# Kernel tuning notes

Hardware: AMD Instinct MI355X
Metric: run time of the kernel (lower is better)

## Reference

```python
import jax, jax.numpy as jnp
import numpy as np

INPUT_DIM, HIDDEN_DIM, N_HEADS, N_AGENTS = 256, 512, 8, 64
BATCH, N_ENTITIES = 128, 256


def setup_inputs() -> dict:
    key = jax.random.key(0)
    ks = jax.random.split(key, 6)
    x = jax.random.normal(ks[0], (BATCH, N_ENTITIES, INPUT_DIM), dtype=jnp.float32)
    # encode: LeakyReLU -> Linear(input_dim, hidden_dim)
    W_enc = jax.random.normal(ks[1], (INPUT_DIM, HIDDEN_DIM), dtype=jnp.float32) * (1.0 / np.sqrt(INPUT_DIM))
    b_enc = jnp.zeros((HIDDEN_DIM,), dtype=jnp.float32)
    # per-head full hidden x hidden projections, stacked on head axis
    WQ = jax.random.normal(ks[2], (N_HEADS, HIDDEN_DIM, HIDDEN_DIM), dtype=jnp.float32)
    WK = jax.random.normal(ks[3], (N_HEADS, HIDDEN_DIM, HIDDEN_DIM), dtype=jnp.float32)
    WV = jax.random.normal(ks[4], (N_HEADS, HIDDEN_DIM, HIDDEN_DIM), dtype=jnp.float32)
    return {"x": x, "W_enc": W_enc, "b_enc": b_enc, "WQ": WQ, "WK": WK, "WV": WV, "n_agents": N_AGENTS}


def reference(x, W_enc, b_enc, WQ, WK, WV, n_agents):
    scale = 1.0 / np.sqrt(WQ.shape[-1]).astype(np.float32)
    # encode: LeakyReLU(0.01) then Linear
    h = jax.nn.leaky_relu(x, negative_slope=0.01) @ W_enc + b_enc  # [b, e, H]
    ha = h[:, :n_agents]  # [b, a, H]
    # all heads at once: n = head axis
    Q = jnp.einsum('bah,nhd->nbad', ha, WQ)
    K = jnp.einsum('beh,nhd->nbed', h, WK)
    V = jnp.einsum('beh,nhd->nbed', h, WV)
    scores = jnp.einsum('nbad,nbed->nbae', Q, K) * scale
    p = jax.nn.softmax(scores, axis=-1)
    # redundant renormalization from the original code
    prob = p / (jnp.sum(p, axis=-1, keepdims=True) + 1e-12)
    z = jnp.einsum('nbae,nbed->nbad', prob, V)  # [n, b, a, H]
    return jnp.mean(z, axis=0)  # [b, a, H]
```

## Files before the change

kernel.cpp:

```cpp
#include <hip/hip_runtime.h>
#include <math.h>

#define BATCH  128
#define NENT   256
#define INDIM  256
#define HID    512
#define NHEAD  8
#define NAGENT 64
#define SCALE  0.04419417382415922f


typedef unsigned short u16;
typedef unsigned int   u32;

typedef __bf16 bf16x8  __attribute__((ext_vector_type(8)));
typedef float  floatx4 __attribute__((ext_vector_type(4)));
typedef u32    u32x4   __attribute__((ext_vector_type(4)));
typedef u32    u32x2   __attribute__((ext_vector_type(2)));

union Frag {
    u32x4 s;
    struct { u32x2 lo, hi; } p;
    bf16x8 v;
};

__device__ __forceinline__ u16 f2bf(float x) {
    u32 u = __float_as_uint(x);
    return (u16)((u + 0x7FFFu + ((u >> 16) & 1u)) >> 16);
}
__device__ __forceinline__ float bf2f(u16 b) {
    return __uint_as_float(((u32)b) << 16);
}
__device__ __forceinline__ void split4(const float4& r, ushort4& hh, ushort4& hl) {
    hh.x = f2bf(r.x); hl.x = f2bf(r.x - bf2f(hh.x));
    hh.y = f2bf(r.y); hl.y = f2bf(r.y - bf2f(hh.y));
    hh.z = f2bf(r.z); hl.z = f2bf(r.z - bf2f(hh.z));
    hh.w = f2bf(r.w); hl.w = f2bf(r.w - bf2f(hh.w));
}

__global__ __launch_bounds__(256) void wenc_t_kernel(const float* __restrict__ W,
                                                     u16* __restrict__ Wt_p) {
    __shared__ float tile[64][68];
    const int bid = blockIdx.x;
    const int k0 = (bid & 3) * 64;
    const int d0 = (bid >> 2) * 64;
    const int t = threadIdx.x;
    const int ki = t >> 2, dc = (t & 3) * 16;
    #pragma unroll
    for (int c = 0; c < 4; ++c)
        *(float4*)&tile[ki][dc + c * 4] =
            *(const float4*)(W + (size_t)(k0 + ki) * HID + d0 + dc + c * 4);
    __syncthreads();
    const int dr = t >> 2, kc = (t & 3) * 16;
    #pragma unroll
    for (int c = 0; c < 4; ++c) {
        float4 v = make_float4(tile[kc + c * 4 + 0][dr], tile[kc + c * 4 + 1][dr],
                               tile[kc + c * 4 + 2][dr], tile[kc + c * 4 + 3][dr]);
        ushort4 hh, hl; split4(v, hh, hl);
        const int kk = k0 + kc + c * 4;
        size_t o = (size_t)(d0 + dr) * 512 + (size_t)(kk >> 5) * 64 + (kk & 31);
        *(ushort4*)(Wt_p + o) = hh;
        *(ushort4*)(Wt_p + o + 32) = hl;
    }
}

__global__ __launch_bounds__(256) void enc_kernel(const float* __restrict__ x,
                                                  const u16* __restrict__ Wt_p,
                                                  const float* __restrict__ bias,
                                                  u16* __restrict__ h_p) {
    __shared__ u16 Ah[32][264];
    __shared__ u16 Al[32][264];
    const int r0 = blockIdx.x * 32;
    const int t  = threadIdx.x;
    {
        const int row = t >> 3;
        const float* xr = x + (size_t)(r0 + row) * INDIM;
        #pragma unroll
        for (int j = 0; j < 8; ++j) {
            const int k0 = ((t & 7) + j * 8) * 4;
            float4 v = *(const float4*)(xr + k0);
            v.x = v.x > 0.f ? v.x : 0.01f * v.x;
            v.y = v.y > 0.f ? v.y : 0.01f * v.y;
            v.z = v.z > 0.f ? v.z : 0.01f * v.z;
            v.w = v.w > 0.f ? v.w : 0.01f * v.w;
            ushort4 hh, hl; split4(v, hh, hl);
            *(ushort4*)&Ah[row][k0] = hh;
            *(ushort4*)&Al[row][k0] = hl;
        }
    }
    __syncthreads();

    const int wid = t >> 6, lane = t & 63, l15 = lane & 15, quad = lane >> 4;
    const int mbase = (wid & 1) * 16;
    const int nbase = (wid >> 1) * 256;
    const floatx4 z4 = {0.f, 0.f, 0.f, 0.f};
    floatx4 acc[16];
    #pragma unroll
    for (int i = 0; i < 16; ++i) acc[i] = z4;

    for (int ks = 0; ks < 8; ++ks) {
        const int k = ks * 32 + quad * 8;
        Frag Afh, Afl;
        Afh.s = *(const u32x4*)&Ah[mbase + l15][k];
        Afl.s = *(const u32x4*)&Al[mbase + l15][k];
        #pragma unroll
        for (int nt = 0; nt < 16; ++nt) {
            const int d = nbase + nt * 16 + l15;
            const size_t wo = (size_t)d * 512 + (size_t)ks * 64 + quad * 8;
            Frag Bh, Bl;
            Bh.s = *(const u32x4*)(Wt_p + wo);
            Bl.s = *(const u32x4*)(Wt_p + wo + 32);
            floatx4 c = acc[nt];
            c = __builtin_amdgcn_mfma_f32_16x16x32_bf16(Afh.v, Bh.v, c, 0, 0, 0);
            c = __builtin_amdgcn_mfma_f32_16x16x32_bf16(Afh.v, Bl.v, c, 0, 0, 0);
            c = __builtin_amdgcn_mfma_f32_16x16x32_bf16(Afl.v, Bh.v, c, 0, 0, 0);
            acc[nt] = c;
        }
    }
    #pragma unroll
    for (int nt = 0; nt < 16; ++nt) {
        const int d = nbase + nt * 16 + l15;
        const float bv = bias[d];
        #pragma unroll
        for (int r = 0; r < 4; ++r) {
            const float v = acc[nt][r] + bv;
            const u16 hi = f2bf(v);
            const u16 lo = f2bf(v - bf2f(hi));
            const size_t o = (size_t)(r0 + mbase + quad * 4 + r) * 1024
                           + (size_t)(d >> 5) * 64 + (d & 31);
            h_p[o]      = hi;
            h_p[o + 32] = lo;
        }
    }
}

__global__ __launch_bounds__(256) void ht_kernel(const u16* __restrict__ h_p,
                                                 u16* __restrict__ hT) {
    __shared__ u16 tile[64][72];
    const int bid = blockIdx.x;
    const int dt = bid & 7;
    const int et = (bid >> 3) & 3;
    const int b  = bid >> 5;
    const int t  = threadIdx.x;
    const int r  = t >> 2, cs = (t & 3) * 16;
    const int dg = dt * 64 + cs;
    const u16* src = h_p + (size_t)(b * 256 + et * 64 + r) * 1024
                   + (size_t)(dg >> 5) * 64 + (dg & 31);
    *(ushort4*)&tile[r][cs + 0]  = *(const ushort4*)(src + 0);
    *(ushort4*)&tile[r][cs + 4]  = *(const ushort4*)(src + 4);
    *(ushort4*)&tile[r][cs + 8]  = *(const ushort4*)(src + 8);
    *(ushort4*)&tile[r][cs + 12] = *(const ushort4*)(src + 12);
    __syncthreads();
    const int d = t >> 2, es = (t & 3) * 16;
    u16* dst = hT + (size_t)b * 131072 + (size_t)(dt * 64 + d) * 256 + et * 64 + es;
    #pragma unroll
    for (int c = 0; c < 4; ++c) {
        ushort4 v = make_ushort4(tile[es + c * 4 + 0][d], tile[es + c * 4 + 1][d],
                                 tile[es + c * 4 + 2][d], tile[es + c * 4 + 3][d]);
        *(ushort4*)(dst + c * 4) = v;
    }
}

__global__ __launch_bounds__(256) void wqk_kernel(const float* __restrict__ WQ,
                                                  const float* __restrict__ WK,
                                                  u16* __restrict__ Mt_p) {
    __shared__ u16 Ah[64][72], Al[64][72], Bh[64][72], Bl[64][72];
    const int bid = blockIdx.x;
    const int jt = (bid & 7) * 64;
    const int it = ((bid >> 3) & 7) * 64;
    const int n  = bid >> 6;
    const float* qp = WQ + (size_t)n * 262144;
    const float* kp = WK + (size_t)n * 262144;
    const int t = threadIdx.x;
    const int wid = t >> 6, lane = t & 63, l15 = lane & 15, quad = lane >> 4;
    const int srow = t >> 2, sc = (t & 3) * 16;

    const floatx4 z4 = {0.f, 0.f, 0.f, 0.f};
    floatx4 acc[4];
    #pragma unroll
    for (int i = 0; i < 4; ++i) acc[i] = z4;

    for (int kc = 0; kc < HID; kc += 64) {
        #pragma unroll
        for (int f = 0; f < 4; ++f) {
            float4 va = *(const float4*)(kp + (size_t)(jt + srow) * HID + kc + sc + f * 4);
            ushort4 hh, hl; split4(va, hh, hl);
            *(ushort4*)&Ah[srow][sc + f * 4] = hh;
            *(ushort4*)&Al[srow][sc + f * 4] = hl;
            float4 vb = *(const float4*)(qp + (size_t)(it + srow) * HID + kc + sc + f * 4);
            split4(vb, hh, hl);
            *(ushort4*)&Bh[srow][sc + f * 4] = hh;
            *(ushort4*)&Bl[srow][sc + f * 4] = hl;
        }
        __syncthreads();
        #pragma unroll
        for (int ks = 0; ks < 2; ++ks) {
            const int k = ks * 32 + quad * 8;
            Frag Afh, Afl;
            Afh.s = *(const u32x4*)&Ah[wid * 16 + l15][k];
            Afl.s = *(const u32x4*)&Al[wid * 16 + l15][k];
            #pragma unroll
            for (int nt = 0; nt < 4; ++nt) {
                Frag Bfh, Bfl;
                Bfh.s = *(const u32x4*)&Bh[nt * 16 + l15][k];
                Bfl.s = *(const u32x4*)&Bl[nt * 16 + l15][k];
                floatx4 c = acc[nt];
                c = __builtin_amdgcn_mfma_f32_16x16x32_bf16(Afh.v, Bfh.v, c, 0, 0, 0);
                c = __builtin_amdgcn_mfma_f32_16x16x32_bf16(Afh.v, Bfl.v, c, 0, 0, 0);
                c = __builtin_amdgcn_mfma_f32_16x16x32_bf16(Afl.v, Bfh.v, c, 0, 0, 0);
                acc[nt] = c;
            }
        }
        __syncthreads();
    }
    #pragma unroll
    for (int nt = 0; nt < 4; ++nt)
        #pragma unroll
        for (int r = 0; r < 4; ++r) {
            const float v = acc[nt][r] * SCALE;
            const u16 hi = f2bf(v);
            const u16 lo = f2bf(v - bf2f(hi));
            const int j = jt + wid * 16 + quad * 4 + r;
            const int i = it + nt * 16 + l15;
            const size_t o = (size_t)n * 524288 + (size_t)j * 1024
                           + (size_t)(i >> 5) * 64 + (i & 31);
            Mt_p[o]      = hi;
            Mt_p[o + 32] = lo;
        }
}

__global__ __launch_bounds__(256) void wvt_kernel(const float* __restrict__ WV,
                                                  u16* __restrict__ WVt) {
    __shared__ float tile[64][68];
    const int bid = blockIdx.x;
    const int i0 = (bid & 7) * 64;
    const int o0 = ((bid >> 3) & 7) * 64;
    const int n  = bid >> 6;
    const float* src = WV + (size_t)n * 262144;
    const int t  = threadIdx.x;
    const int di = t >> 2;
    const int dc = (t & 3) * 16;
    #pragma unroll
    for (int c = 0; c < 4; ++c)
        *(float4*)&tile[di][dc + c * 4] =
            *(const float4*)(src + (size_t)(i0 + di) * HID + o0 + dc + c * 4);
    __syncthreads();
    const int dr = t >> 2;
    const int ic = (t & 3) * 16;
    size_t o = (size_t)n * 262144 + (size_t)(o0 + dr) * HID + i0 + ic;
    #pragma unroll
    for (int c = 0; c < 4; ++c) {
        ushort4 v = make_ushort4(f2bf(tile[ic + c * 4 + 0][dr]), f2bf(tile[ic + c * 4 + 1][dr]),
                                 f2bf(tile[ic + c * 4 + 2][dr]), f2bf(tile[ic + c * 4 + 3][dr]));
        *(ushort4*)(WVt + o + c * 4) = v;
    }
}

template<bool USE_HT>
__global__ __launch_bounds__(256, 3) void attn_kernel(const u16* __restrict__ h_p,
                                                      const u16* __restrict__ Mt_p,
                                                      const u16* __restrict__ WVt,
                                                      const u16* __restrict__ hT,
                                                      float* __restrict__ out) {
    __shared__ __align__(16) char SM[53504];
    u16*   Th  = (u16*)SM;
    u16*   Tl  = (u16*)(SM + 16640);
    float* S   = (float*)SM;
    float* red = (float*)(SM + 33792);
    u16*   HbT = (u16*)SM;
    u16*   U   = (u16*)SM;
    u16*   Pt  = (u16*)(SM + 36864);

    const int bid = blockIdx.x;
    const int x7 = bid & 7;
    const int s  = bid >> 3;
    const int at = s & 1;
    const int n  = (x7 >> 1) | (((s >> 1) & 1) << 2);
    const int b  = ((s >> 2) << 1) | (x7 & 1);

    const int tid  = threadIdx.x;
    const int wid  = tid >> 6;
    const int lane = tid & 63;
    const int l15  = lane & 15;
    const int quad = lane >> 4;

    const u16* Mtp = Mt_p + (size_t)n * 524288;
    const u16* Wv  = WVt  + (size_t)n * 262144;
    const u16* hTb = hT + (size_t)b * 131072;
    const size_t hb_base = (size_t)b * 262144;
    const size_t ha_row0 = hb_base + (size_t)(at * 32) * 1024;

    const floatx4 z4 = {0.f, 0.f, 0.f, 0.f};
    floatx4 Sacc[8];
    #pragma unroll
    for (int i = 0; i < 8; ++i) Sacc[i] = z4;

    for (int H = 0; H < 2; ++H) {
        floatx4 Tacc[8];
        #pragma unroll
        for (int i = 0; i < 8; ++i) Tacc[i] = z4;
        for (int ks = 0; ks < 16; ++ks) {
            const int ko = ks * 64 + quad * 8;
            Frag Ahf[2], Alf[2];
            #pragma unroll
            for (int mt = 0; mt < 2; ++mt) {
                const size_t ro = ha_row0 + (size_t)(mt * 16 + l15) * 1024 + ko;
                Ahf[mt].s = *(const u32x4*)(h_p + ro);
                Alf[mt].s = *(const u32x4*)(h_p + ro + 32);
            }
            #pragma unroll
            for (int nt = 0; nt < 4; ++nt) {
                const int d = H * 256 + (wid * 4 + nt) * 16 + l15;
                const size_t mo = (size_t)d * 1024 + ko;
                Frag Bh, Bl;
                Bh.s = *(const u32x4*)(Mtp + mo);
                Bl.s = *(const u32x4*)(Mtp + mo + 32);
                #pragma unroll
                for (int mt = 0; mt < 2; ++mt) {
                    floatx4 c = Tacc[mt * 4 + nt];
                    c = __builtin_amdgcn_mfma_f32_16x16x32_bf16(Ahf[mt].v, Bh.v, c, 0, 0, 0);
                    c = __builtin_amdgcn_mfma_f32_16x16x32_bf16(Ahf[mt].v, Bl.v, c, 0, 0, 0);
                    c = __builtin_amdgcn_mfma_f32_16x16x32_bf16(Alf[mt].v, Bh.v, c, 0, 0, 0);
                    Tacc[mt * 4 + nt] = c;
                }
            }
        }
        __syncthreads();
        #pragma unroll
        for (int mt = 0; mt < 2; ++mt)
            #pragma unroll
            for (int nt = 0; nt < 4; ++nt)
                #pragma unroll
                for (int r = 0; r < 4; ++r) {
                    const float v = Tacc[mt * 4 + nt][r];
                    const int a  = mt * 16 + quad * 4 + r;
                    const int dl = (wid * 4 + nt) * 16 + l15;
                    const u16 hi = f2bf(v);
                    Th[a * 260 + dl] = hi;
                    Tl[a * 260 + dl] = f2bf(v - bf2f(hi));
                }
        __syncthreads();
        for (int ks = 0; ks < 8; ++ks) {
            const int kl = ks * 32 + quad * 8;
            const int ko = (H * 8 + ks) * 64 + quad * 8;
            Frag Ahf[4], Alf[4];
            #pragma unroll
            for (int mt = 0; mt < 4; ++mt) {
                const size_t ro = hb_base + (size_t)((wid * 4 + mt) * 16 + l15) * 1024 + ko;
                Ahf[mt].s = *(const u32x4*)(h_p + ro);
                Alf[mt].s = *(const u32x4*)(h_p + ro + 32);
            }
            #pragma unroll
            for (int nt = 0; nt < 2; ++nt) {
                const int ac = nt * 16 + l15;
                Frag Bfh, Bfl;
                Bfh.p.lo = *(const u32x2*)(Th + ac * 260 + kl);
                Bfh.p.hi = *(const u32x2*)(Th + ac * 260 + kl + 4);
                Bfl.p.lo = *(const u32x2*)(Tl + ac * 260 + kl);
                Bfl.p.hi = *(const u32x2*)(Tl + ac * 260 + kl + 4);
                #pragma unroll
                for (int mt = 0; mt < 4; ++mt) {
                    floatx4 c = Sacc[mt * 2 + nt];
                    c = __builtin_amdgcn_mfma_f32_16x16x32_bf16(Ahf[mt].v, Bfh.v, c, 0, 0, 0);
                    c = __builtin_amdgcn_mfma_f32_16x16x32_bf16(Ahf[mt].v, Bfl.v, c, 0, 0, 0);
                    c = __builtin_amdgcn_mfma_f32_16x16x32_bf16(Alf[mt].v, Bfh.v, c, 0, 0, 0);
                    Sacc[mt * 2 + nt] = c;
                }
            }
        }
    }
    __syncthreads();
    #pragma unroll
    for (int mt = 0; mt < 4; ++mt)
        #pragma unroll
        for (int nt = 0; nt < 2; ++nt)
            #pragma unroll
            for (int r = 0; r < 4; ++r) {
                const int e = (wid * 4 + mt) * 16 + quad * 4 + r;
                const int a = nt * 16 + l15;
                S[e * 33 + a] = Sacc[mt * 2 + nt][r];
            }
    __syncthreads();
    {
        const int a   = tid & 31;
        const int seg = tid >> 5;
        float v[32];
        #pragma unroll
        for (int i = 0; i < 32; ++i) v[i] = S[(seg * 32 + i) * 33 + a];
        float mx = v[0];
        #pragma unroll
        for (int i = 1; i < 32; ++i) mx = fmaxf(mx, v[i]);
        red[a * 8 + seg] = mx;
        __syncthreads();
        float gmx = red[a * 8 + 0];
        #pragma unroll
        for (int i = 1; i < 8; ++i) gmx = fmaxf(gmx, red[a * 8 + i]);
        __syncthreads();
        float sum = 0.f;
        #pragma unroll
        for (int i = 0; i < 32; ++i) { v[i] = expf(v[i] - gmx); sum += v[i]; }
        red[a * 8 + seg] = sum;
        __syncthreads();
        float tot = 0.f;
        #pragma unroll
        for (int i = 0; i < 8; ++i) tot += red[a * 8 + i];
        const float inv = 1.0f / tot;
        #pragma unroll
        for (int i = 0; i < 32; ++i)
            Pt[a * 260 + seg * 32 + i] = f2bf(v[i] * inv);
    }
    __syncthreads();
    floatx4 Uacc[16];
    #pragma unroll
    for (int i = 0; i < 16; ++i) Uacc[i] = z4;
    const int d0w = wid * 128;
    if (USE_HT) {
        for (int ep = 0; ep < 4; ++ep) {
            Frag Bc[2][8];
            #pragma unroll
            for (int sb = 0; sb < 2; ++sb)
                #pragma unroll
                for (int dt = 0; dt < 8; ++dt) {
                    const int d = d0w + dt * 16 + l15;
                    Bc[sb][dt].s = *(const u32x4*)(hTb + (size_t)d * 256
                                                   + (2 * ep + sb) * 32 + quad * 8);
                }
            #pragma unroll
            for (int sb = 0; sb < 2; ++sb) {
                const int et = 2 * ep + sb;
                Frag Ap[2];
                #pragma unroll
                for (int mt = 0; mt < 2; ++mt) {
                    const int ar = mt * 16 + l15;
                    Ap[mt].p.lo = *(const u32x2*)(Pt + ar * 260 + et * 32 + quad * 8);
                    Ap[mt].p.hi = *(const u32x2*)(Pt + ar * 260 + et * 32 + quad * 8 + 4);
                }
                #pragma unroll
                for (int dt = 0; dt < 8; ++dt)
                    #pragma unroll
                    for (int mt = 0; mt < 2; ++mt)
                        Uacc[mt * 8 + dt] = __builtin_amdgcn_mfma_f32_16x16x32_bf16(
                            Ap[mt].v, Bc[sb][dt].v, Uacc[mt * 8 + dt], 0, 0, 0);
            }
        }
    } else {
        u32* Hb32 = (u32*)HbT;
        for (int et = 0; et < 8; ++et) {
            {
                const int epi = lane & 15;
                const int q   = lane >> 4;
                const size_t r0p = hb_base + (size_t)(et * 32 + 2 * epi) * 1024;
                #pragma unroll
                for (int c = 0; c < 4; ++c) {
                    const int d0 = d0w + c * 32 + q * 8;
                    const size_t po = (size_t)(d0 >> 5) * 64 + (d0 & 31);
                    u32x4 u0 = *(const u32x4*)(h_p + r0p + po);
                    u32x4 u1 = *(const u32x4*)(h_p + r0p + 1024 + po);
                    #pragma unroll
                    for (int p = 0; p < 4; ++p) {
                        const u32 w0 = (u0[p] & 0xFFFFu) | (u1[p] << 16);
                        const u32 w1 = (u0[p] >> 16) | (u1[p] & 0xFFFF0000u);
                        Hb32[(d0 + 2 * p) * 18 + epi]     = w0;
                        Hb32[(d0 + 2 * p + 1) * 18 + epi] = w1;
                    }
                }
            }
            Frag Ap[2];
            #pragma unroll
            for (int mt = 0; mt < 2; ++mt) {
                const int ar = mt * 16 + l15;
                Ap[mt].p.lo = *(const u32x2*)(Pt + ar * 260 + et * 32 + quad * 8);
                Ap[mt].p.hi = *(const u32x2*)(Pt + ar * 260 + et * 32 + quad * 8 + 4);
            }
            #pragma unroll
            for (int dt = 0; dt < 8; ++dt) {
                const int d = d0w + dt * 16 + l15;
                Frag Bf;
                Bf.p.lo = *(const u32x2*)(HbT + d * 36 + quad * 8);
                Bf.p.hi = *(const u32x2*)(HbT + d * 36 + quad * 8 + 4);
                #pragma unroll
                for (int mt = 0; mt < 2; ++mt)
                    Uacc[mt * 8 + dt] = __builtin_amdgcn_mfma_f32_16x16x32_bf16(
                        Ap[mt].v, Bf.v, Uacc[mt * 8 + dt], 0, 0, 0);
            }
        }
    }
    __syncthreads();
    #pragma unroll
    for (int mt = 0; mt < 2; ++mt)
        #pragma unroll
        for (int dt = 0; dt < 8; ++dt)
            #pragma unroll
            for (int r = 0; r < 4; ++r) {
                const int a = mt * 16 + quad * 4 + r;
                const int d = d0w + dt * 16 + l15;
                U[a * 520 + d] = f2bf(Uacc[mt * 8 + dt][r]);
            }
    __syncthreads();
    floatx4 Zacc[16];
    #pragma unroll
    for (int i = 0; i < 16; ++i) Zacc[i] = z4;
    for (int kp = 0; kp < 8; ++kp) {
        Frag Bw[2][8];
        #pragma unroll
        for (int sb = 0; sb < 2; ++sb) {
            const int k = (kp * 2 + sb) * 32 + quad * 8;
            #pragma unroll
            for (int dt = 0; dt < 8; ++dt) {
                const int dn = (wid * 8 + dt) * 16 + l15;
                Bw[sb][dt].s = *(const u32x4*)(Wv + (size_t)dn * HID + k);
            }
        }
        #pragma unroll
        for (int sb = 0; sb < 2; ++sb) {
            const int k = (kp * 2 + sb) * 32 + quad * 8;
            Frag Au[2];
            #pragma unroll
            for (int mt = 0; mt < 2; ++mt) {
                Au[mt].p.lo = *(const u32x2*)(U + (mt * 16 + l15) * 520 + k);
                Au[mt].p.hi = *(const u32x2*)(U + (mt * 16 + l15) * 520 + k + 4);
            }
            #pragma unroll
            for (int dt = 0; dt < 8; ++dt)
                #pragma unroll
                for (int mt = 0; mt < 2; ++mt)
                    Zacc[mt * 8 + dt] = __builtin_amdgcn_mfma_f32_16x16x32_bf16(
                        Au[mt].v, Bw[sb][dt].v, Zacc[mt * 8 + dt], 0, 0, 0);
        }
    }
    float* ob = out + ((size_t)b * NAGENT + at * 32) * HID;
    #pragma unroll
    for (int mt = 0; mt < 2; ++mt)
        #pragma unroll
        for (int dt = 0; dt < 8; ++dt)
            #pragma unroll
            for (int r = 0; r < 4; ++r) {
                const int a  = mt * 16 + quad * 4 + r;
                const int dn = (wid * 8 + dt) * 16 + l15;
                atomicAdd(ob + (size_t)a * HID + dn, Zacc[mt * 8 + dt][r] * 0.125f);
            }
}

extern "C" void kernel_launch(void* const* d_in, const int* in_sizes, int n_in,
                              void* d_out, int out_size, void* d_ws, size_t ws_size,
                              hipStream_t stream) {
    const float* x     = (const float*)d_in[0];
    const float* W_enc = (const float*)d_in[1];
    const float* b_enc = (const float*)d_in[2];
    const float* WQ    = (const float*)d_in[3];
    const float* WK    = (const float*)d_in[4];
    const float* WV    = (const float*)d_in[5];
    float* out = (float*)d_out;

    char* ws = (char*)d_ws;
    u16* h_p  = (u16*)ws;
    u16* Mt_p = (u16*)(ws + 67108864);
    u16* WVt  = (u16*)(ws + 75497472);
    u16* hT   = (u16*)(ws + 79691776);
    u16* Wt_p = WVt;

    const bool useHT = ws_size >= (size_t)113246208;

    hipMemsetAsync(d_out, 0, (size_t)out_size * sizeof(float), stream);
    wenc_t_kernel<<<32, 256, 0, stream>>>(W_enc, Wt_p);
    enc_kernel<<<1024, 256, 0, stream>>>(x, Wt_p, b_enc, h_p);
    if (useHT) ht_kernel<<<4096, 256, 0, stream>>>(h_p, hT);
    wvt_kernel<<<512, 256, 0, stream>>>(WV, WVt);
    wqk_kernel<<<512, 256, 0, stream>>>(WQ, WK, Mt_p);
    if (useHT)
        attn_kernel<true><<<2048, 256, 0, stream>>>(h_p, Mt_p, WVt, hT, out);
    else
        attn_kernel<false><<<2048, 256, 0, stream>>>(h_p, Mt_p, WVt, hT, out);
}
```

Baseline: 967.1 us.

## Store operands in MFMA-fragment chunk layout and double-buffer via global_load_lds

Intermediate buffers (h, M^T, W_V, h^T) are rewritten in a 16-row chunked layout that matches MFMA fragment order, so each fragment load becomes a contiguous 16-byte access. The attention kernel now streams B operands into per-wave LDS staging buffers with global_load_lds in a double-buffered pipeline using waitcnt, and splits the T and U stages into quarters to fit LDS. The goal is to cut strided global loads and hide memory latency, at the cost of more LDS pressure, more barriers and more complex index math.

```diff
diff --git a/kernel.cpp b/kernel.cpp
--- a/kernel.cpp
+++ b/kernel.cpp
@@ -24,6 +24,15 @@
     bf16x8 v;
 };
 
+#define MFMA(a, b, c) __builtin_amdgcn_mfma_f32_16x16x32_bf16((a), (b), (c), 0, 0, 0)
+#define VMW(n) (((n) & 0xF) | (0xF << 8) | (0x7 << 4))
+
+__device__ __forceinline__ void gld16(const u16* g, u16* l) {
+    __builtin_amdgcn_global_load_lds(
+        (const __attribute__((address_space(1))) void*)g,
+        (__attribute__((address_space(3))) void*)l, 16, 0, 0);
+}
+
 __device__ __forceinline__ u16 f2bf(float x) {
     u32 u = __float_as_uint(x);
     return (u16)((u + 0x7FFFu + ((u >> 16) & 1u)) >> 16);
@@ -36,6 +45,9 @@
     hh.y = f2bf(r.y); hl.y = f2bf(r.y - bf2f(hh.y));
     hh.z = f2bf(r.z); hl.z = f2bf(r.z - bf2f(hh.z));
     hh.w = f2bf(r.w); hl.w = f2bf(r.w - bf2f(hh.w));
+}
+__device__ __forceinline__ size_t chunk_off(int row16, int col) {
+    return (size_t)((col >> 3) & 3) * 128 + (size_t)row16 * 8 + (col & 7);
 }
 
 __global__ __launch_bounds__(256) void wenc_t_kernel(const float* __restrict__ W,
@@ -67,7 +79,7 @@
 __global__ __launch_bounds__(256) void enc_kernel(const float* __restrict__ x,
                                                   const u16* __restrict__ Wt_p,
                                                   const float* __restrict__ bias,
-                                                  u16* __restrict__ h_p) {
+                                                  u16* __restrict__ hC) {
     __shared__ u16 Ah[32][264];
     __shared__ u16 Al[32][264];
     const int r0 = blockIdx.x * 32;
@@ -111,9 +123,9 @@
             Bh.s = *(const u32x4*)(Wt_p + wo);
             Bl.s = *(const u32x4*)(Wt_p + wo + 32);
             floatx4 c = acc[nt];
-            c = __builtin_amdgcn_mfma_f32_16x16x32_bf16(Afh.v, Bh.v, c, 0, 0, 0);
-            c = __builtin_amdgcn_mfma_f32_16x16x32_bf16(Afh.v, Bl.v, c, 0, 0, 0);
-            c = __builtin_amdgcn_mfma_f32_16x16x32_bf16(Afl.v, Bh.v, c, 0, 0, 0);
+            c = MFMA(Afh.v, Bh.v, c);
+            c = MFMA(Afh.v, Bl.v, c);
+            c = MFMA(Afl.v, Bh.v, c);
             acc[nt] = c;
         }
     }
@@ -126,44 +138,49 @@
             const float v = acc[nt][r] + bv;
             const u16 hi = f2bf(v);
             const u16 lo = f2bf(v - bf2f(hi));
-            const size_t o = (size_t)(r0 + mbase + quad * 4 + r) * 1024
-                           + (size_t)(d >> 5) * 64 + (d & 31);
-            h_p[o]      = hi;
-            h_p[o + 32] = lo;
-        }
-    }
-}
-
-__global__ __launch_bounds__(256) void ht_kernel(const u16* __restrict__ h_p,
-                                                 u16* __restrict__ hT) {
+            const int row = r0 + mbase + quad * 4 + r;
+            const size_t o = (size_t)((row >> 4) * 16 + (d >> 5)) * 1024
+                           + chunk_off(row & 15, d);
+            hC[o]       = hi;
+            hC[o + 512] = lo;
+        }
+    }
+}
+
+__global__ __launch_bounds__(256) void ht_kernel(const u16* __restrict__ hC,
+                                                 u16* __restrict__ hTC) {
     __shared__ u16 tile[64][72];
     const int bid = blockIdx.x;
-    const int dt = bid & 7;
-    const int et = (bid >> 3) & 3;
-    const int b  = bid >> 5;
-    const int t  = threadIdx.x;
+    const int dt64 = bid & 7;
+    const int et64 = (bid >> 3) & 3;
+    const int b    = bid >> 5;
+    const int t    = threadIdx.x;
     const int r  = t >> 2, cs = (t & 3) * 16;
-    const int dg = dt * 64 + cs;
-    const u16* src = h_p + (size_t)(b * 256 + et * 64 + r) * 1024
-                   + (size_t)(dg >> 5) * 64 + (dg & 31);
-    *(ushort4*)&tile[r][cs + 0]  = *(const ushort4*)(src + 0);
-    *(ushort4*)&tile[r][cs + 4]  = *(const ushort4*)(src + 4);
-    *(ushort4*)&tile[r][cs + 8]  = *(const ushort4*)(src + 8);
-    *(ushort4*)&tile[r][cs + 12] = *(const ushort4*)(src + 12);
+    const int row = b * 256 + et64 * 64 + r;
+    #pragma unroll
+    for (int c = 0; c < 4; ++c) {
+        const int d0 = dt64 * 64 + cs + c * 4;
+        const size_t o = (size_t)((row >> 4) * 16 + (d0 >> 5)) * 1024
+                       + chunk_off(row & 15, d0);
+        *(ushort4*)&tile[r][cs + c * 4] = *(const ushort4*)(hC + o);
+    }
     __syncthreads();
-    const int d = t >> 2, es = (t & 3) * 16;
-    u16* dst = hT + (size_t)b * 131072 + (size_t)(dt * 64 + d) * 256 + et * 64 + es;
+    const int dr = t >> 2, es = (t & 3) * 16;
+    const int dg = dt64 * 64 + dr;
     #pragma unroll
     for (int c = 0; c < 4; ++c) {
-        ushort4 v = make_ushort4(tile[es + c * 4 + 0][d], tile[es + c * 4 + 1][d],
-                                 tile[es + c * 4 + 2][d], tile[es + c * 4 + 3][d]);
-        *(ushort4*)(dst + c * 4) = v;
+        const int e = et64 * 64 + es + c * 4;
+        ushort4 v = make_ushort4(tile[es + c * 4 + 0][dr], tile[es + c * 4 + 1][dr],
+                                 tile[es + c * 4 + 2][dr], tile[es + c * 4 + 3][dr]);
+        const size_t o = (size_t)((b * 32 + (dg >> 4)) * 8 + (e >> 5)) * 512
+                       + (size_t)((e >> 3) & 3) * 128 + (size_t)(dg & 15) * 8 + (e & 7);
+        *(ushort4*)(hTC + o) = v;
     }
 }
 
 __global__ __launch_bounds__(256) void wqk_kernel(const float* __restrict__ WQ,
                                                   const float* __restrict__ WK,
-                                                  u16* __restrict__ Mt_p) {
+                                                  u16* __restrict__ MtC) {
     __shared__ u16 Ah[64][72], Al[64][72], Bh[64][72], Bl[64][72];
     const int bid = blockIdx.x;
     const int jt = (bid & 7) * 64;
@@ -205,9 +222,9 @@
                 Bfh.s = *(const u32x4*)&Bh[nt * 16 + l15][k];
                 Bfl.s = *(const u32x4*)&Bl[nt * 16 + l15][k];
                 floatx4 c = acc[nt];
-                c = __builtin_amdgcn_mfma_f32_16x16x32_bf16(Afh.v, Bfh.v, c, 0, 0, 0);
-                c = __builtin_amdgcn_mfma_f32_16x16x32_bf16(Afh.v, Bfl.v, c, 0, 0, 0);
-                c = __builtin_amdgcn_mfma_f32_16x16x32_bf16(Afl.v, Bfh.v, c, 0, 0, 0);
+                c = MFMA(Afh.v, Bfh.v, c);
+                c = MFMA(Afh.v, Bfl.v, c);
+                c = MFMA(Afl.v, Bfh.v, c);
                 acc[nt] = c;
             }
         }
@@ -222,15 +239,16 @@
             const u16 lo = f2bf(v - bf2f(hi));
             const int j = jt + wid * 16 + quad * 4 + r;
             const int i = it + nt * 16 + l15;
-            const size_t o = (size_t)n * 524288 + (size_t)j * 1024
-                           + (size_t)(i >> 5) * 64 + (i & 31);
-            Mt_p[o]      = hi;
-            Mt_p[o + 32] = lo;
+            const size_t o = (size_t)n * 524288
+                           + (size_t)((j >> 4) * 16 + (i >> 5)) * 1024
+                           + chunk_off(j & 15, i);
+            MtC[o]       = hi;
+            MtC[o + 512] = lo;
         }
 }
 
 __global__ __launch_bounds__(256) void wvt_kernel(const float* __restrict__ WV,
-                                                  u16* __restrict__ WVt) {
+                                                  u16* __restrict__ WvC) {
     __shared__ float tile[64][68];
     const int bid = blockIdx.x;
     const int i0 = (bid & 7) * 64;
@@ -247,29 +265,31 @@
     __syncthreads();
     const int dr = t >> 2;
     const int ic = (t & 3) * 16;
-    size_t o = (size_t)n * 262144 + (size_t)(o0 + dr) * HID + i0 + ic;
+    const int dn = o0 + dr;
     #pragma unroll
     for (int c = 0; c < 4; ++c) {
+        const int k = i0 + ic + c * 4;
         ushort4 v = make_ushort4(f2bf(tile[ic + c * 4 + 0][dr]), f2bf(tile[ic + c * 4 + 1][dr]),
                                  f2bf(tile[ic + c * 4 + 2][dr]), f2bf(tile[ic + c * 4 + 3][dr]));
-        *(ushort4*)(WVt + o + c * 4) = v;
+        const size_t o = (size_t)((n * 32 + (dn >> 4)) * 16 + (k >> 5)) * 512
+                       + (size_t)((k >> 3) & 3) * 128 + (size_t)(dn & 15) * 8 + (k & 7);
+        *(ushort4*)(WvC + o) = v;
     }
 }
 
 template<bool USE_HT>
-__global__ __launch_bounds__(256, 3) void attn_kernel(const u16* __restrict__ h_p,
-                                                      const u16* __restrict__ Mt_p,
-                                                      const u16* __restrict__ WVt,
-                                                      const u16* __restrict__ hT,
+__global__ __launch_bounds__(256, 3) void attn_kernel(const u16* __restrict__ hC,
+                                                      const u16* __restrict__ MtC_g,
+                                                      const u16* __restrict__ WvC_g,
+                                                      const u16* __restrict__ hTC,
                                                       float* __restrict__ out) {
     __shared__ __align__(16) char SM[53504];
-    u16*   Th  = (u16*)SM;
-    u16*   Tl  = (u16*)(SM + 16640);
     float* S   = (float*)SM;
     float* red = (float*)(SM + 33792);
+    u16*   Uq  = (u16*)(SM + 34816);
+    u16*   Tq  = (u16*)(SM + 36864);
+    u16*   Pt  = (u16*)(SM + 36864);
     u16*   HbT = (u16*)SM;
-    u16*   U   = (u16*)SM;
-    u16*   Pt  = (u16*)(SM + 36864);
 
     const int bid = blockIdx.x;
     const int x7 = bid & 7;
@@ -284,92 +304,136 @@
     const int l15  = lane & 15;
     const int quad = lane >> 4;
 
-    const u16* Mtp = Mt_p + (size_t)n * 524288;
-    const u16* Wv  = WVt  + (size_t)n * 262144;
-    const u16* hTb = hT + (size_t)b * 131072;
-    const size_t hb_base = (size_t)b * 262144;
-    const size_t ha_row0 = hb_base + (size_t)(at * 32) * 1024;
+    u16* stg = (u16*)(SM + wid * 8192);
+
+    const u16* MtC = MtC_g + (size_t)n * 524288;
+    const u16* WvC = WvC_g + (size_t)n * 262144;
+    const int  rtA = b * 16 + at * 2;
 
     const floatx4 z4 = {0.f, 0.f, 0.f, 0.f};
     floatx4 Sacc[8];
     #pragma unroll
     for (int i = 0; i < 8; ++i) Sacc[i] = z4;
 
-    for (int H = 0; H < 2; ++H) {
-        floatx4 Tacc[8];
-        #pragma unroll
-        for (int i = 0; i < 8; ++i) Tacc[i] = z4;
+    for (int qtr = 0; qtr < 4; ++qtr) {
+        floatx4 Tacc[4] = {z4, z4, z4, z4};
+        Frag Aq[2][4];
+        auto dmaA = [&](int ks, int bsel) {
+            u16* dst = stg + bsel * 2048;
+            #pragma unroll
+            for (int nt = 0; nt < 2; ++nt) {
+                const u16* src = MtC + (size_t)((qtr * 8 + wid * 2 + nt) * 16 + ks) * 1024;
+                gld16(src + lane * 8,       dst + nt * 1024 + lane * 8);
+                gld16(src + 512 + lane * 8, dst + nt * 1024 + 512 + lane * 8);
+            }
+        };
+        auto ldA = [&](int ks, Frag* A) {
+            #pragma unroll
+            for (int mt = 0; mt < 2; ++mt) {
+                const u16* src = hC + (size_t)((rtA + mt) * 16 + ks) * 1024
+                               + quad * 128 + l15 * 8;
+                A[mt * 2 + 0].s = *(const u32x4*)src;
+                A[mt * 2 + 1].s = *(const u32x4*)(src + 512);
+            }
+        };
+        dmaA(0, 0);
+        __builtin_amdgcn_wave_barrier();
+        ldA(0, Aq[0]);
+        __builtin_amdgcn_wave_barrier();
+        #pragma unroll 2
         for (int ks = 0; ks < 16; ++ks) {
-            const int ko = ks * 64 + quad * 8;
+            const int bsel = ks & 1;
+            if (ks < 15) {
+                dmaA(ks + 1, bsel ^ 1);
+                __builtin_amdgcn_wave_barrier();
+                ldA(ks + 1, Aq[bsel ^ 1]);
+                __builtin_amdgcn_wave_barrier();
+                __builtin_amdgcn_s_waitcnt(VMW(8));
+            } else {
+                __builtin_amdgcn_s_waitcnt(VMW(0));
+            }
+            __builtin_amdgcn_wave_barrier();
+            const u16* buf = stg + bsel * 2048;
+            #pragma unroll
+            for (int nt = 0; nt < 2; ++nt) {
+                Frag Bh, Bl;
+                Bh.s = *(const u32x4*)(buf + nt * 1024 + quad * 128 + l15 * 8);
+                Bl.s = *(const u32x4*)(buf + nt * 1024 + 512 + quad * 128 + l15 * 8);
+                #pragma unroll
+                for (int mt = 0; mt < 2; ++mt) {
+                    floatx4 c = Tacc[mt * 2 + nt];
+                    c = MFMA(Aq[bsel][mt * 2 + 0].v, Bh.v, c);
+                    c = MFMA(Aq[bsel][mt * 2 + 0].v, Bl.v, c);
+                    c = MFMA(Aq[bsel][mt * 2 + 1].v, Bh.v, c);
+                    Tacc[mt * 2 + nt] = c;
+                }
+            }
+        }
+        __syncthreads();
+        #pragma unroll
+        for (int mt = 0; mt < 2; ++mt)
+            #pragma unroll
+            for (int nt = 0; nt < 2; ++nt)
+                #pragma unroll
+                for (int r = 0; r < 4; ++r) {
+                    const float v = Tacc[mt * 2 + nt][r];
+                    const int a   = mt * 16 + quad * 4 + r;
+                    const int col = (wid * 2 + nt) * 16 + l15;
+                    const u16 hi = f2bf(v);
+                    Tq[a * 260 + (col >> 5) * 64 + (col & 31)]      = hi;
+                    Tq[a * 260 + (col >> 5) * 64 + (col & 31) + 32] = f2bf(v - bf2f(hi));
+                }
+        __syncthreads();
+        auto dmaB = [&](int st, int bsel) {
+            const int ks = st >> 1, h = st & 1;
+            u16* dst = stg + bsel * 2048;
+            #pragma unroll
+            for (int i = 0; i < 2; ++i) {
+                const int rt = b * 16 + wid * 4 + h * 2 + i;
+                const u16* src = hC + (size_t)(rt * 16 + qtr * 4 + ks) * 1024;
+                gld16(src + lane * 8,       dst + i * 1024 + lane * 8);
+                gld16(src + 512 + lane * 8, dst + i * 1024 + 512 + lane * 8);
+            }
+        };
+        dmaB(0, 0);
+        #pragma unroll 2
+        for (int st = 0; st < 8; ++st) {
+            const int bsel = st & 1;
+            if (st < 7) {
+                dmaB(st + 1, bsel ^ 1);
+                __builtin_amdgcn_s_waitcnt(VMW(4));
+            } else {
+                __builtin_amdgcn_s_waitcnt(VMW(0));
+            }
+            __builtin_amdgcn_wave_barrier();
+            const int ks = st >> 1, h = st & 1;
+            const u16* buf = stg + bsel * 2048;
             Frag Ahf[2], Alf[2];
             #pragma unroll
-            for (int mt = 0; mt < 2; ++mt) {
-                const size_t ro = ha_row0 + (size_t)(mt * 16 + l15) * 1024 + ko;
-                Ahf[mt].s = *(const u32x4*)(h_p + ro);
-                Alf[mt].s = *(const u32x4*)(h_p + ro + 32);
-            }
-            #pragma unroll
-            for (int nt = 0; nt < 4; ++nt) {
-                const int d = H * 256 + (wid * 4 + nt) * 16 + l15;
-                const size_t mo = (size_t)d * 1024 + ko;
-                Frag Bh, Bl;
-                Bh.s = *(const u32x4*)(Mtp + mo);
-                Bl.s = *(const u32x4*)(Mtp + mo + 32);
-                #pragma unroll
-                for (int mt = 0; mt < 2; ++mt) {
-                    floatx4 c = Tacc[mt * 4 + nt];
-                    c = __builtin_amdgcn_mfma_f32_16x16x32_bf16(Ahf[mt].v, Bh.v, c, 0, 0, 0);
-                    c = __builtin_amdgcn_mfma_f32_16x16x32_bf16(Ahf[mt].v, Bl.v, c, 0, 0, 0);
-                    c = __builtin_amdgcn_mfma_f32_16x16x32_bf16(Alf[mt].v, Bh.v, c, 0, 0, 0);
-                    Tacc[mt * 4 + nt] = c;
-                }
-            }
-        }
-        __syncthreads();
-        #pragma unroll
-        for (int mt = 0; mt < 2; ++mt)
-            #pragma unroll
-            for (int nt = 0; nt < 4; ++nt)
-                #pragma unroll
-                for (int r = 0; r < 4; ++r) {
-                    const float v = Tacc[mt * 4 + nt][r];
-                    const int a  = mt * 16 + quad * 4 + r;
-                    const int dl = (wid * 4 + nt) * 16 + l15;
-                    const u16 hi = f2bf(v);
-                    Th[a * 260 + dl] = hi;
-                    Tl[a * 260 + dl] = f2bf(v - bf2f(hi));
-                }
-        __syncthreads();
-        for (int ks = 0; ks < 8; ++ks) {
-            const int kl = ks * 32 + quad * 8;
-            const int ko = (H * 8 + ks) * 64 + quad * 8;
-            Frag Ahf[4], Alf[4];
-            #pragma unroll
-            for (int mt = 0; mt < 4; ++mt) {
-                const size_t ro = hb_base + (size_t)((wid * 4 + mt) * 16 + l15) * 1024 + ko;
-                Ahf[mt].s = *(const u32x4*)(h_p + ro);
-                Alf[mt].s = *(const u32x4*)(h_p + ro + 32);
+            for (int i = 0; i < 2; ++i) {
+                Ahf[i].s = *(const u32x4*)(buf + i * 1024 + quad * 128 + l15 * 8);
+                Alf[i].s = *(const u32x4*)(buf + i * 1024 + 512 + quad * 128 + l15 * 8);
             }
             #pragma unroll
             for (int nt = 0; nt < 2; ++nt) {
                 const int ac = nt * 16 + l15;
                 Frag Bfh, Bfl;
-                Bfh.p.lo = *(const u32x2*)(Th + ac * 260 + kl);
-                Bfh.p.hi = *(const u32x2*)(Th + ac * 260 + kl + 4);
-                Bfl.p.lo = *(const u32x2*)(Tl + ac * 260 + kl);
-                Bfl.p.hi = *(const u32x2*)(Tl + ac * 260 + kl + 4);
-                #pragma unroll
-                for (int mt = 0; mt < 4; ++mt) {
-                    floatx4 c = Sacc[mt * 2 + nt];
-                    c = __builtin_amdgcn_mfma_f32_16x16x32_bf16(Ahf[mt].v, Bfh.v, c, 0, 0, 0);
-                    c = __builtin_amdgcn_mfma_f32_16x16x32_bf16(Ahf[mt].v, Bfl.v, c, 0, 0, 0);
-                    c = __builtin_amdgcn_mfma_f32_16x16x32_bf16(Alf[mt].v, Bfh.v, c, 0, 0, 0);
-                    Sacc[mt * 2 + nt] = c;
+                Bfh.p.lo = *(const u32x2*)(Tq + ac * 260 + ks * 64 + quad * 8);
+                Bfh.p.hi = *(const u32x2*)(Tq + ac * 260 + ks * 64 + quad * 8 + 4);
+                Bfl.p.lo = *(const u32x2*)(Tq + ac * 260 + ks * 64 + quad * 8 + 32);
+                Bfl.p.hi = *(const u32x2*)(Tq + ac * 260 + ks * 64 + quad * 8 + 36);
+                #pragma unroll
+                for (int i = 0; i < 2; ++i) {
+                    floatx4 c = Sacc[(h * 2 + i) * 2 + nt];
+                    c = MFMA(Ahf[i].v, Bfh.v, c);
+                    c = MFMA(Ahf[i].v, Bfl.v, c);
+                    c = MFMA(Alf[i].v, Bfh.v, c);
+                    Sacc[(h * 2 + i) * 2 + nt] = c;
                 }
             }
         }
-    }
-    __syncthreads();
+        __syncthreads();
+    }
     #pragma unroll
     for (int mt = 0; mt < 4; ++mt)
         #pragma unroll
@@ -415,32 +479,42 @@
     for (int i = 0; i < 16; ++i) Uacc[i] = z4;
     const int d0w = wid * 128;
     if (USE_HT) {
-        for (int ep = 0; ep < 4; ++ep) {
-            Frag Bc[2][8];
-            #pragma unroll
-            for (int sb = 0; sb < 2; ++sb)
-                #pragma unroll
-                for (int dt = 0; dt < 8; ++dt) {
-                    const int d = d0w + dt * 16 + l15;
-                    Bc[sb][dt].s = *(const u32x4*)(hTb + (size_t)d * 256
-                                                   + (2 * ep + sb) * 32 + quad * 8);
-                }
-            #pragma unroll
-            for (int sb = 0; sb < 2; ++sb) {
-                const int et = 2 * ep + sb;
-                Frag Ap[2];
-                #pragma unroll
-                for (int mt = 0; mt < 2; ++mt) {
-                    const int ar = mt * 16 + l15;
-                    Ap[mt].p.lo = *(const u32x2*)(Pt + ar * 260 + et * 32 + quad * 8);
-                    Ap[mt].p.hi = *(const u32x2*)(Pt + ar * 260 + et * 32 + quad * 8 + 4);
-                }
-                #pragma unroll
-                for (int dt = 0; dt < 8; ++dt)
-                    #pragma unroll
-                    for (int mt = 0; mt < 2; ++mt)
-                        Uacc[mt * 8 + dt] = __builtin_amdgcn_mfma_f32_16x16x32_bf16(
-                            Ap[mt].v, Bc[sb][dt].v, Uacc[mt * 8 + dt], 0, 0, 0);
+        auto dmaC = [&](int st, int bsel) {
+            const int et = st >> 1, h = st & 1;
+            u16* dst = stg + bsel * 2048;
+            #pragma unroll
+            for (int i = 0; i < 4; ++i) {
+                const u16* src = hTC + (size_t)((b * 32 + wid * 8 + h * 4 + i) * 8 + et) * 512;
+                gld16(src + lane * 8, dst + i * 512 + lane * 8);
+            }
+        };
+        dmaC(0, 0);
+        #pragma unroll 2
+        for (int st = 0; st < 16; ++st) {
+            const int bsel = st & 1;
+            if (st < 15) {
+                dmaC(st + 1, bsel ^ 1);
+                __builtin_amdgcn_s_waitcnt(VMW(4));
+            } else {
+                __builtin_amdgcn_s_waitcnt(VMW(0));
+            }
+            __builtin_amdgcn_wave_barrier();
+            const int et = st >> 1, h = st & 1;
+            const u16* buf = stg + bsel * 2048;
+            Frag Ap[2];
+            #pragma unroll
+            for (int mt = 0; mt < 2; ++mt) {
+                const int ar = mt * 16 + l15;
+                Ap[mt].p.lo = *(const u32x2*)(Pt + ar * 260 + et * 32 + quad * 8);
+                Ap[mt].p.hi = *(const u32x2*)(Pt + ar * 260 + et * 32 + quad * 8 + 4);
+            }
+            #pragma unroll
+            for (int i = 0; i < 4; ++i) {
+                Frag Bf;
+                Bf.s = *(const u32x4*)(buf + i * 512 + quad * 128 + l15 * 8);
+                #pragma unroll
+                for (int mt = 0; mt < 2; ++mt)
+                    Uacc[mt * 8 + h * 4 + i] = MFMA(Ap[mt].v, Bf.v, Uacc[mt * 8 + h * 4 + i]);
             }
         }
     } else {
@@ -448,14 +522,18 @@
         for (int et = 0; et < 8; ++et) {
             {
                 const int epi = lane & 15;
-                const int q   = lane >> 4;
-                const size_t r0p = hb_base + (size_t)(et * 32 + 2 * epi) * 1024;
+                const int q8  = lane >> 4;
                 #pragma unroll
                 for (int c = 0; c < 4; ++c) {
-                    const int d0 = d0w + c * 32 + q * 8;
-                    const size_t po = (size_t)(d0 >> 5) * 64 + (d0 & 31);
-                    u32x4 u0 = *(const u32x4*)(h_p + r0p + po);
-                    u32x4 u1 = *(const u32x4*)(h_p + r0p + 1024 + po);
+                    const int d0 = d0w + c * 32 + q8 * 8;
+                    const int row0 = et * 32 + 2 * epi;
+                    const size_t o0 = (size_t)((b * 16 + (row0 >> 4)) * 16 + (d0 >> 5)) * 1024
+                                    + chunk_off(row0 & 15, d0);
+                    const int row1 = row0 + 1;
+                    const size_t o1 = (size_t)((b * 16 + (row1 >> 4)) * 16 + (d0 >> 5)) * 1024
+                                    + chunk_off(row1 & 15, d0);
+                    u32x4 u0 = *(const u32x4*)(hC + o0);
+                    u32x4 u1 = *(const u32x4*)(hC + o1);
                     #pragma unroll
                     for (int p = 0; p < 4; ++p) {
                         const u32 w0 = (u0[p] & 0xFFFFu) | (u1[p] << 16);
@@ -480,52 +558,65 @@
                 Bf.p.hi = *(const u32x2*)(HbT + d * 36 + quad * 8 + 4);
                 #pragma unroll
                 for (int mt = 0; mt < 2; ++mt)
-                    Uacc[mt * 8 + dt] = __builtin_amdgcn_mfma_f32_16x16x32_bf16(
-                        Ap[mt].v, Bf.v, Uacc[mt * 8 + dt], 0, 0, 0);
-            }
-        }
-    }
-    __syncthreads();
-    #pragma unroll
-    for (int mt = 0; mt < 2; ++mt)
-        #pragma unroll
-        for (int dt = 0; dt < 8; ++dt)
-            #pragma unroll
-            for (int r = 0; r < 4; ++r) {
-                const int a = mt * 16 + quad * 4 + r;
-                const int d = d0w + dt * 16 + l15;
-                U[a * 520 + d] = f2bf(Uacc[mt * 8 + dt][r]);
-            }
-    __syncthreads();
+                    Uacc[mt * 8 + dt] = MFMA(Ap[mt].v, Bf.v, Uacc[mt * 8 + dt]);
+            }
+        }
+    }
     floatx4 Zacc[16];
     #pragma unroll
     for (int i = 0; i < 16; ++i) Zacc[i] = z4;
-    for (int kp = 0; kp < 8; ++kp) {
-        Frag Bw[2][8];
-        #pragma unroll
-        for (int sb = 0; sb < 2; ++sb) {
-            const int k = (kp * 2 + sb) * 32 + quad * 8;
-            #pragma unroll
-            for (int dt = 0; dt < 8; ++dt) {
-                const int dn = (wid * 8 + dt) * 16 + l15;
-                Bw[sb][dt].s = *(const u32x4*)(Wv + (size_t)dn * HID + k);
-            }
-        }
-        #pragma unroll
-        for (int sb = 0; sb < 2; ++sb) {
-            const int k = (kp * 2 + sb) * 32 + quad * 8;
+    for (int qq = 0; qq < 4; ++qq) {
+        __syncthreads();
+        if (wid == qq) {
+            #pragma unroll
+            for (int mt = 0; mt < 2; ++mt)
+                #pragma unroll
+                for (int dt = 0; dt < 8; ++dt)
+                    #pragma unroll
+                    for (int r = 0; r < 4; ++r) {
+                        const int a   = mt * 16 + quad * 4 + r;
+                        const int col = dt * 16 + l15;
+                        Uq[a * 132 + col] = f2bf(Uacc[mt * 8 + dt][r]);
+                    }
+        }
+        __syncthreads();
+        auto dmaD = [&](int st, int bsel) {
+            const int ksl = st >> 1, h = st & 1;
+            u16* dst = stg + bsel * 2048;
+            #pragma unroll
+            for (int i = 0; i < 4; ++i) {
+                const u16* src = WvC + (size_t)((wid * 8 + h * 4 + i) * 16 + qq * 4 + ksl) * 512;
+                gld16(src + lane * 8, dst + i * 512 + lane * 8);
+            }
+        };
+        dmaD(0, 0);
+        #pragma unroll 2
+        for (int st = 0; st < 8; ++st) {
+            const int bsel = st & 1;
+            if (st < 7) {
+                dmaD(st + 1, bsel ^ 1);
+                __builtin_amdgcn_s_waitcnt(VMW(4));
+            } else {
+                __builtin_amdgcn_s_waitcnt(VMW(0));
+            }
+            __builtin_amdgcn_wave_barrier();
+            const int ksl = st >> 1, h = st & 1;
+            const u16* buf = stg + bsel * 2048;
             Frag Au[2];
             #pragma unroll
             for (int mt = 0; mt < 2; ++mt) {
-                Au[mt].p.lo = *(const u32x2*)(U + (mt * 16 + l15) * 520 + k);
-                Au[mt].p.hi = *(const u32x2*)(U + (mt * 16 + l15) * 520 + k + 4);
-            }
-            #pragma unroll
-            for (int dt = 0; dt < 8; ++dt)
+                const int ar = mt * 16 + l15;
+                Au[mt].p.lo = *(const u32x2*)(Uq + ar * 132 + ksl * 32 + quad * 8);
+                Au[mt].p.hi = *(const u32x2*)(Uq + ar * 132 + ksl * 32 + quad * 8 + 4);
+            }
+            #pragma unroll
+            for (int i = 0; i < 4; ++i) {
+                Frag Bf;
+                Bf.s = *(const u32x4*)(buf + i * 512 + quad * 128 + l15 * 8);
                 #pragma unroll
                 for (int mt = 0; mt < 2; ++mt)
-                    Zacc[mt * 8 + dt] = __builtin_amdgcn_mfma_f32_16x16x32_bf16(
-                        Au[mt].v, Bw[sb][dt].v, Zacc[mt * 8 + dt], 0, 0, 0);
+                    Zacc[mt * 8 + h * 4 + i] = MFMA(Au[mt].v, Bf.v, Zacc[mt * 8 + h * 4 + i]);
+            }
         }
     }
     float* ob = out + ((size_t)b * NAGENT + at * 32) * HID;
@@ -553,22 +644,22 @@
     float* out = (float*)d_out;
 
     char* ws = (char*)d_ws;
-    u16* h_p  = (u16*)ws;
-    u16* Mt_p = (u16*)(ws + 67108864);
-    u16* WVt  = (u16*)(ws + 75497472);
-    u16* hT   = (u16*)(ws + 79691776);
-    u16* Wt_p = WVt;
+    u16* hC   = (u16*)ws;
+    u16* MtC  = (u16*)(ws + 67108864);
+    u16* WvC  = (u16*)(ws + 75497472);
+    u16* hTC  = (u16*)(ws + 79691776);
+    u16* Wt_p = WvC;
 
     const bool useHT = ws_size >= (size_t)113246208;
 
     hipMemsetAsync(d_out, 0, (size_t)out_size * sizeof(float), stream);
     wenc_t_kernel<<<32, 256, 0, stream>>>(W_enc, Wt_p);
-    enc_kernel<<<1024, 256, 0, stream>>>(x, Wt_p, b_enc, h_p);
-    if (useHT) ht_kernel<<<4096, 256, 0, stream>>>(h_p, hT);
-    wvt_kernel<<<512, 256, 0, stream>>>(WV, WVt);
-    wqk_kernel<<<512, 256, 0, stream>>>(WQ, WK, Mt_p);
+    enc_kernel<<<1024, 256, 0, stream>>>(x, Wt_p, b_enc, hC);
+    if (useHT) ht_kernel<<<4096, 256, 0, stream>>>(hC, hTC);
+    wvt_kernel<<<512, 256, 0, stream>>>(WV, WvC);
+    wqk_kernel<<<512, 256, 0, stream>>>(WQ, WK, MtC);
     if (useHT)
-        attn_kernel<true><<<2048, 256, 0, stream>>>(h_p, Mt_p, WVt, hT, out);
+        attn_kernel<true><<<2048, 256, 0, stream>>>(hC, MtC, WvC, hTC, out);
     else
-        attn_kernel<false><<<2048, 256, 0, stream>>>(h_p, Mt_p, WVt, hT, out);
-}
+        attn_kernel<false><<<2048, 256, 0, stream>>>(hC, MtC, WvC, hTC, out);
+}
```

After: 2.203 ms. 2.28x slower.
